# Kernel tuning notes

Hardware: AMD Instinct MI355X
Metric: run time of the kernel (lower is better)

Reference implementation:

```python
import jax, jax.numpy as jnp
import numpy as np

B, S, H, M, T = 64, 512, 768, 512, 26


def setup_inputs() -> dict:
    key = jax.random.key(0)
    ks = jax.random.split(key, 10)
    hidden = jax.random.normal(ks[0], (B, S, H), dtype=jnp.float32)
    W1 = jax.random.normal(ks[1], (M, H), dtype=jnp.float32) * 0.02
    b1 = jnp.zeros((M,), jnp.float32)
    W2 = jax.random.normal(ks[2], (T, M), dtype=jnp.float32) * 0.02
    b2 = jnp.zeros((T,), jnp.float32)
    start_trans = jax.random.normal(ks[3], (T,), dtype=jnp.float32) * 0.1
    end_trans = jax.random.normal(ks[4], (T,), dtype=jnp.float32) * 0.1
    trans = jax.random.normal(ks[5], (T, T), dtype=jnp.float32) * 0.1
    labels = jax.random.randint(ks[6], (B, S), 0, T, dtype=jnp.int32)
    lengths = jax.random.randint(ks[7], (B,), 1, S + 1, dtype=jnp.int32)
    return dict(hidden=hidden, W1=W1, b1=b1, W2=W2, b2=b2,
                start_trans=start_trans, end_trans=end_trans, trans=trans,
                labels=labels, lengths=lengths)


def _crf_nll(emissions, labels, lengths, start_trans, end_trans, trans):
    # emissions: [B,S,T]; labels: [B,S]; lengths: [B]
    maskf = (jnp.arange(S)[None, :] < lengths[:, None]).astype(emissions.dtype)  # [B,S]

    # --- numerator: score of the gold path (torchcrf _compute_score) ---
    emit_gold = jnp.take_along_axis(emissions, labels[..., None], axis=-1)[..., 0]  # [B,S]
    trans_gold = trans[labels[:, :-1], labels[:, 1:]]  # [B,S-1]
    last_tags = jnp.take_along_axis(labels, (lengths - 1)[:, None], axis=1)[:, 0]  # [B]
    numerator = (start_trans[labels[:, 0]] + emit_gold[:, 0]
                 + jnp.sum((trans_gold + emit_gold[:, 1:]) * maskf[:, 1:], axis=1)
                 + end_trans[last_tags])  # [B]

    # --- denominator: log partition via forward algorithm (lax.scan) ---
    alpha0 = start_trans[None, :] + emissions[:, 0]  # [B,T]
    emis_t = jnp.swapaxes(emissions[:, 1:], 0, 1)    # [S-1,B,T]
    mask_t = jnp.swapaxes(maskf[:, 1:] > 0, 0, 1)    # [S-1,B] bool

    def step(alpha, xs):
        emit, m = xs
        # alpha[b,i] + trans[i,j] + emit[b,j] -> logsumexp over i
        nxt = jax.nn.logsumexp(alpha[:, :, None] + trans[None, :, :] + emit[:, None, :], axis=1)
        return jnp.where(m[:, None], nxt, alpha), None

    alpha, _ = jax.lax.scan(step, alpha0, (emis_t, mask_t))
    denominator = jax.nn.logsumexp(alpha + end_trans[None, :], axis=1)  # [B]

    llh = numerator - denominator
    return -jnp.mean(llh)  # loss = -crf(..., reduction='mean')


def reference(hidden, W1, b1, W2, b2, start_trans, end_trans, trans, labels, lengths):
    h = jnp.einsum('bsh,mh->bsm', hidden, W1) + b1      # fc1 (no activation in source)
    emissions = jnp.einsum('bsm,tm->bst', h, W2) + b2   # fc2 -> [B,S,T]
    return _crf_nll(emissions, labels, lengths, start_trans, end_trans, trans)
```

## Files before the change

### kernel.cpp

```cpp
#include <hip/hip_runtime.h>
#include <math.h>

#define Bn 64
#define Sn 512
#define Hn 768
#define Mn 512
#define Tn 26
#define TP 32

#define OFF_BC    0
#define OFF_BFRAG 32
#define OFF_EX    (32 + 12288)
#define EXSZ      ((size_t)Bn*Sn*TP)
#define OFF_ACC   (OFF_EX + EXSZ)
#define OFF_CNT   (OFF_ACC + 1)

typedef __attribute__((ext_vector_type(8)))  short bfrag;
typedef __attribute__((ext_vector_type(4)))  float f32x4;
typedef __attribute__((ext_vector_type(16))) float f32x16;

__device__ __forceinline__ short f2bf(float f) {
    unsigned u = __float_as_uint(f);
    unsigned r = (u + 0x7FFFu + ((u >> 16) & 1u)) >> 16;
    return (short)r;
}
__device__ __forceinline__ unsigned cvtpk(float a, float b) {
    unsigned r;
    asm("v_cvt_pk_bf16_f32 %0, %1, %2" : "=v"(r) : "v"(a), "v"(b));
    return r;
}
__device__ __forceinline__ void pswap(unsigned &a, unsigned &b) {
    asm("v_permlane32_swap_b32 %0, %1" : "+v"(a), "+v"(b));
}
__device__ __forceinline__ bfrag mkfrag(unsigned a, unsigned b, unsigned c, unsigned d) {
    union { unsigned u[4]; bfrag v; } x;
    x.u[0] = a; x.u[1] = b; x.u[2] = c; x.u[3] = d;
    return x.v;
}
__device__ __forceinline__ float rl(float x, int i) {
    return __uint_as_float(__builtin_amdgcn_readlane(__float_as_uint(x), i));
}

__global__ __launch_bounds__(256) void k_prep(const float* __restrict__ W1,
                                              const float* __restrict__ b1,
                                              const float* __restrict__ W2,
                                              const float* __restrict__ b2,
                                              float* __restrict__ ws) {
    const int bx = blockIdx.x;
    const int tid = threadIdx.x;
    if (bx == 48) {
        if (tid == 0) {
            ws[OFF_ACC] = 0.f;
            ((unsigned*)ws)[OFF_CNT] = 0u;
        }
        if (tid < TP) {
            float bcv = 0.f;
            if (tid < Tn) {
                float a0 = 0.f, a1 = 0.f, a2 = 0.f, a3 = 0.f;
                const float4* w2 = reinterpret_cast<const float4*>(W2 + (size_t)tid * Mn);
                const float4* bb = reinterpret_cast<const float4*>(b1);
                for (int m = 0; m < Mn / 4; ++m) {
                    float4 w = w2[m], v = bb[m];
                    a0 = fmaf(w.x, v.x, a0); a1 = fmaf(w.y, v.y, a1);
                    a2 = fmaf(w.z, v.z, a2); a3 = fmaf(w.w, v.w, a3);
                }
                bcv = b2[tid] + (a0 + a1) + (a2 + a3);
            }
            ws[OFF_BC + tid] = bcv;
        }
        return;
    }

    __shared__ float mrg[3][64][8];
    const int lane = tid & 63;
    const int wv   = tid >> 6;
    const int k0   = bx * 16;
    const int colA = lane & 15;
    const int mj   = ((lane >> 4) & 3) * 8;

    f32x4 acc0 = {0.f, 0.f, 0.f, 0.f}, acc1 = {0.f, 0.f, 0.f, 0.f};
    for (int mq = 0; mq < 4; ++mq) {
        const int m0 = wv * 128 + mq * 32;
        bfrag av, bv0, bv1;
#pragma unroll
        for (int j = 0; j < 8; ++j)
            av[j] = f2bf(W1[(size_t)(m0 + mj + j) * Hn + k0 + colA]);
        {
            const float* p = W2 + (size_t)(lane & 15) * Mn + m0 + mj;
            float4 x = *reinterpret_cast<const float4*>(p);
            float4 y = *reinterpret_cast<const float4*>(p + 4);
            bv0 = mkfrag(cvtpk(x.x, x.y), cvtpk(x.z, x.w), cvtpk(y.x, y.y), cvtpk(y.z, y.w));
        }
        {
            int c = 16 + (lane & 15);
            bfrag z = {};
            if (c < Tn) {
                const float* p = W2 + (size_t)c * Mn + m0 + mj;
                float4 x = *reinterpret_cast<const float4*>(p);
                float4 y = *reinterpret_cast<const float4*>(p + 4);
                z = mkfrag(cvtpk(x.x, x.y), cvtpk(x.z, x.w), cvtpk(y.x, y.y), cvtpk(y.z, y.w));
            }
            bv1 = z;
        }
        acc0 = __builtin_amdgcn_mfma_f32_16x16x32_bf16(av, bv0, acc0, 0, 0, 0);
        acc1 = __builtin_amdgcn_mfma_f32_16x16x32_bf16(av, bv1, acc1, 0, 0, 0);
    }

    if (wv > 0) {
#pragma unroll
        for (int i = 0; i < 4; ++i) {
            mrg[wv - 1][lane][i]     = acc0[i];
            mrg[wv - 1][lane][4 + i] = acc1[i];
        }
    }
    __syncthreads();
    if (wv == 0) {
        unsigned short* Bfo = (unsigned short*)(ws + OFF_BFRAG);
#pragma unroll
        for (int i = 0; i < 4; ++i) {
            float v0 = acc0[i] + mrg[0][lane][i]     + mrg[1][lane][i]     + mrg[2][lane][i];
            float v1 = acc1[i] + mrg[0][lane][4 + i] + mrg[1][lane][4 + i] + mrg[2][lane][4 + i];
            int k   = k0 + ((lane >> 4) & 3) * 4 + i;
            int ks2 = k >> 5;
            int fl  = ((k >> 3) & 3) * 16 + (lane & 15);
            Bfo[((size_t)(ks2 * 2 + 0) * 64 + fl) * 8 + (k & 7)] = (unsigned short)f2bf(v0);
            Bfo[((size_t)(ks2 * 2 + 1) * 64 + fl) * 8 + (k & 7)] = (unsigned short)f2bf(v1);
        }
    }
}

#define LOADK(KS, FA, FB, BV0, BV1)                                                        \
    {                                                                                      \
        const float* ap = abase + (KS) * 32;                                               \
        FA = *reinterpret_cast<const float4*>(ap);                                         \
        FB = *reinterpret_cast<const float4*>(ap + 4);                                     \
        BV0 = *reinterpret_cast<const bfrag*>(Bf + ((size_t)((KS) * 2 + 0) * 64 + l) * 8); \
        BV1 = *reinterpret_cast<const bfrag*>(Bf + ((size_t)((KS) * 2 + 1) * 64 + l) * 8); \
    }

__global__ __launch_bounds__(64, 2) void k_gemm(const float* __restrict__ hidden,
                                                const float* __restrict__ ws,
                                                float* __restrict__ Eexp) {
    const int l    = threadIdx.x;
    const int row0 = blockIdx.x * 16;
    const int arow = row0 + (l & 15);
    const int kg   = l >> 4;
    const float* abase = hidden + (size_t)arow * Hn + kg * 8;
    const unsigned short* Bf = (const unsigned short*)(ws + OFF_BFRAG);

    f32x4 acc0 = {0.f, 0.f, 0.f, 0.f}, acc1 = {0.f, 0.f, 0.f, 0.f};

    float4 fa0, fb0, fa1, fb1;
    bfrag bv00, bv01, bv10, bv11;
    LOADK(0, fa0, fb0, bv00, bv01);
    LOADK(1, fa1, fb1, bv10, bv11);

#pragma unroll 1
    for (int ks = 0; ks < 24; ks += 2) {
        float4 ta, tb; bfrag t0, t1;
        if (ks + 2 < 24) LOADK(ks + 2, ta, tb, t0, t1);
        bfrag av = mkfrag(cvtpk(fa0.x, fa0.y), cvtpk(fa0.z, fa0.w),
                          cvtpk(fb0.x, fb0.y), cvtpk(fb0.z, fb0.w));
        acc0 = __builtin_amdgcn_mfma_f32_16x16x32_bf16(av, bv00, acc0, 0, 0, 0);
        acc1 = __builtin_amdgcn_mfma_f32_16x16x32_bf16(av, bv01, acc1, 0, 0, 0);
        fa0 = ta; fb0 = tb; bv00 = t0; bv01 = t1;

        float4 ua, ub; bfrag u0, u1;
        if (ks + 3 < 24) LOADK(ks + 3, ua, ub, u0, u1);
        av = mkfrag(cvtpk(fa1.x, fa1.y), cvtpk(fa1.z, fa1.w),
                    cvtpk(fb1.x, fb1.y), cvtpk(fb1.z, fb1.w));
        acc0 = __builtin_amdgcn_mfma_f32_16x16x32_bf16(av, bv10, acc0, 0, 0, 0);
        acc1 = __builtin_amdgcn_mfma_f32_16x16x32_bf16(av, bv11, acc1, 0, 0, 0);
        fa1 = ua; fb1 = ub; bv10 = u0; bv11 = u1;
    }

    const int c0 = l & 15;
    const int rbase = row0 + kg * 4;
    float bc0 = ws[OFF_BC + c0], bc1 = ws[OFF_BC + 16 + c0];
#pragma unroll
    for (int i = 0; i < 4; ++i) {
        Eexp[(size_t)(rbase + i) * TP + c0]      = __expf(acc0[i] + bc0);
        Eexp[(size_t)(rbase + i) * TP + 16 + c0] = __expf(acc1[i] + bc1);
    }
}

__global__ __launch_bounds__(1024) void k_scan(const float* __restrict__ Eexp,
                                               const float* __restrict__ start_t,
                                               const float* __restrict__ end_t,
                                               const float* __restrict__ trans,
                                               const int* __restrict__ labels,
                                               const int* __restrict__ lengths,
                                               float* __restrict__ accp,
                                               unsigned* __restrict__ cntp,
                                               float* __restrict__ out) {
    __shared__ float Ech[16][32][32];
    __shared__ unsigned Qp[16][16][32];
    const int tid  = threadIdx.x;
    const int b    = blockIdx.x;
    const int len  = lengths[b];
    const int wv   = tid >> 6;
    const int lane = tid & 63;
    const int t    = lane & 31;
    const int h    = lane >> 5;

    {
        const float* Eb = Eexp + (size_t)b * Sn * TP;
        int lr = lane >> 1, hf = lane & 1;
        int s = wv * 32 + 1 + lr; s = s > 511 ? 511 : s;
        const float4* src = reinterpret_cast<const float4*>(Eb + (size_t)s * TP + hf * 16);
        float4* dst = reinterpret_cast<float4*>(&Ech[wv][lr][hf * 16]);
        dst[0] = src[0]; dst[1] = src[1]; dst[2] = src[2]; dst[3] = src[3];
    }
    __syncthreads();

    {
        const int c  = wv;
        const int s0 = c * 32;
        int nact = len - 1 - s0;
        nact = nact < 0 ? 0 : (nact > 32 ? 32 : nact);

        bfrag A0, A1, B0, B1;
#pragma unroll
        for (int j = 0; j < 8; ++j) {
            int k0 = 8 * h + j, k1 = 16 + 8 * h + j;
            A0[j] = (t < Tn && k0 < Tn) ? f2bf(__expf(trans[k0 * Tn + t]) * 0.03125f) : (short)0;
            A1[j] = (t < Tn && k1 < Tn) ? f2bf(__expf(trans[k1 * Tn + t]) * 0.03125f) : (short)0;
            B0[j] = (k0 == t) ? (short)0x3F80 : (short)0;
            B1[j] = (k1 == t) ? (short)0x3F80 : (short)0;
        }

        float qf[16];
#pragma unroll
        for (int r = 0; r < 16; ++r) {
            int row = (r & 3) + 8 * (r >> 2) + 4 * h;
            qf[r] = (row == t) ? 1.f : 0.f;
        }

        for (int j = 0; j < nact; ++j) {
            f32x16 acc = {};
            acc = __builtin_amdgcn_mfma_f32_32x32x16_bf16(A0, B0, acc, 0, 0, 0);
            acc = __builtin_amdgcn_mfma_f32_32x32x16_bf16(A1, B1, acc, 0, 0, 0);
            const float* ep = &Ech[c][j][4 * h];
            float4 e0 = *reinterpret_cast<const float4*>(ep);
            float4 e1 = *reinterpret_cast<const float4*>(ep + 8);
            float4 e2 = *reinterpret_cast<const float4*>(ep + 16);
            float4 e3 = *reinterpret_cast<const float4*>(ep + 24);
            float ev[16];
            ev[0]  = e0.x; ev[1]  = e0.y; ev[2]  = e0.z; ev[3]  = e0.w;
            ev[4]  = e1.x; ev[5]  = e1.y; ev[6]  = e1.z; ev[7]  = e1.w;
            ev[8]  = e2.x; ev[9]  = e2.y; ev[10] = e2.z; ev[11] = e2.w;
            ev[12] = e3.x; ev[13] = e3.y; ev[14] = e3.z; ev[15] = e3.w;
#pragma unroll
            for (int r = 0; r < 16; ++r) qf[r] = acc[r] * ev[r];
            if (j + 1 < nact) {
                unsigned W0 = cvtpk(qf[0],  qf[1]),  W1 = cvtpk(qf[2],  qf[3]);
                unsigned W2 = cvtpk(qf[4],  qf[5]),  W3 = cvtpk(qf[6],  qf[7]);
                unsigned W4 = cvtpk(qf[8],  qf[9]),  W5 = cvtpk(qf[10], qf[11]);
                unsigned W6 = cvtpk(qf[12], qf[13]), W7 = cvtpk(qf[14], qf[15]);
                pswap(W0, W2); pswap(W1, W3); pswap(W4, W6); pswap(W5, W7);
                B0 = mkfrag(W0, W1, W2, W3);
                B1 = mkfrag(W4, W5, W6, W7);
            }
        }

#pragma unroll
        for (int g = 0; g < 4; ++g) {
            unsigned u0 = cvtpk(qf[4*g + 0], qf[4*g + 1]);
            unsigned u1 = cvtpk(qf[4*g + 2], qf[4*g + 3]);
            Qp[c][4*g + 2*h][t]     = u0;
            Qp[c][4*g + 2*h + 1][t] = u1;
        }
    }
    __syncthreads();

    if (wv == 0) {
        float alpha = (t < Tn) ? __expf(start_t[t]) * Eexp[(size_t)b * Sn * TP + t] : 0.f;
        float logZ = 0.f;
        for (int c = 0; c < 16; ++c) {
            float p0 = 0.f, p1 = 0.f, p2 = 0.f, p3 = 0.f;
#pragma unroll
            for (int p = 0; p < 16; p += 2) {
                unsigned ua = Qp[c][p][t];
                unsigned ub = Qp[c][p + 1][t];
                p0 = fmaf(rl(alpha, 2*p    ), __uint_as_float(ua << 16),          p0);
                p1 = fmaf(rl(alpha, 2*p + 1), __uint_as_float(ua & 0xFFFF0000u), p1);
                p2 = fmaf(rl(alpha, 2*p + 2), __uint_as_float(ub << 16),          p2);
                p3 = fmaf(rl(alpha, 2*p + 3), __uint_as_float(ub & 0xFFFF0000u), p3);
            }
            float v = (p0 + p1) + (p2 + p3);
            float C = __uint_as_float(__builtin_amdgcn_readfirstlane(__float_as_uint(v)));
            alpha = v / C;
            logZ += __logf(C);
        }
        float dv = (t < Tn && lane < 32) ? alpha * __expf(end_t[t]) : 0.f;
#pragma unroll
        for (int off = 32; off; off >>= 1) dv += __shfl_xor(dv, off);
        if (lane == 0) {
            float denom = logZ + __logf(dv) + (float)(len - 1) * 3.46573590279973f;
            atomicAdd(accp, -denom);
            __threadfence();
            unsigned old = atomicAdd(cntp, 1u);
            if (old == 2u * Bn - 1u) {
                float tot = atomicAdd(accp, 0.0f);
                out[0] = -tot * (1.0f / 64.0f);
            }
        }
    } else if (wv == 1) {
        const int base = b * Sn;
        float part = 0.f;
        for (int s2 = 1 + lane; s2 < len; s2 += 64) {
            int lp = labels[base + s2 - 1];
            int lc = labels[base + s2];
            int si = s2 - 1;
            part += trans[lp * Tn + lc] + __logf(Ech[si >> 5][si & 31][lc]);
        }
#pragma unroll
        for (int off = 32; off; off >>= 1) part += __shfl_xor(part, off);
        if (lane == 0) {
            int l0 = labels[base], ll = labels[base + len - 1];
            float numer = part + start_t[l0] + __logf(Eexp[(size_t)base * TP + l0]) + end_t[ll];
            atomicAdd(accp, numer);
            __threadfence();
            unsigned old = atomicAdd(cntp, 1u);
            if (old == 2u * Bn - 1u) {
                float tot = atomicAdd(accp, 0.0f);
                out[0] = -tot * (1.0f / 64.0f);
            }
        }
    }
}

extern "C" void kernel_launch(void* const* d_in, const int* in_sizes, int n_in,
                              void* d_out, int out_size, void* d_ws, size_t ws_size,
                              hipStream_t stream) {
    const float* hidden  = (const float*)d_in[0];
    const float* W1      = (const float*)d_in[1];
    const float* b1      = (const float*)d_in[2];
    const float* W2      = (const float*)d_in[3];
    const float* b2      = (const float*)d_in[4];
    const float* start_t = (const float*)d_in[5];
    const float* end_t   = (const float*)d_in[6];
    const float* trans   = (const float*)d_in[7];
    const int*   labels  = (const int*)d_in[8];
    const int*   lengths = (const int*)d_in[9];
    float* ws  = (float*)d_ws;
    float* out = (float*)d_out;

    hipLaunchKernelGGL(k_prep, dim3(49), dim3(256), 0, stream, W1, b1, W2, b2, ws);
    hipLaunchKernelGGL(k_gemm, dim3(2048), dim3(64), 0, stream, hidden, ws, ws + OFF_EX);
    hipLaunchKernelGGL(k_scan, dim3(64), dim3(1024), 0, stream, ws + OFF_EX, start_t, end_t,
                       trans, labels, lengths, ws + OFF_ACC,
                       (unsigned*)(ws + OFF_CNT), out);
}
```

Measured before the change: 53.62 us.

## Deepen GEMM prefetch pipeline to four stages and parallelize bias fold reduction

The GEMM main loop now keeps four k-steps of A and B fragments in flight instead of two, issuing each next load right after the MFMA that consumes the previous buffer. Past the end of K it reloads step 0 unconditionally rather than branching. This is meant to hide global-load latency for a memory-bound, low-occupancy kernel, at the cost of more registers and some redundant tail loads. Separately, the bias-fold block in the prep kernel spreads the W2·b1 dot products across all 256 threads and combines them with a shuffle and shared memory, where before only 26 threads did serial loops.

```diff
diff --git a/kernel.cpp b/kernel.cpp
--- a/kernel.cpp
+++ b/kernel.cpp
@@ -49,23 +49,37 @@
     const int bx = blockIdx.x;
     const int tid = threadIdx.x;
     if (bx == 48) {
+        __shared__ float part[4][32];
         if (tid == 0) {
             ws[OFF_ACC] = 0.f;
             ((unsigned*)ws)[OFF_CNT] = 0u;
         }
+        const int c = tid & 31;
+        const int w = tid >> 6;
+        const int cl = (tid >> 5) & 1;
+        float a0 = 0.f, a1 = 0.f;
+        if (c < Tn) {
+            const int m0 = w * 128 + cl * 64;
+            const float4* w2 = reinterpret_cast<const float4*>(W2 + (size_t)c * Mn + m0);
+            const float4* bb = reinterpret_cast<const float4*>(b1 + m0);
+#pragma unroll
+            for (int m = 0; m < 16; m += 2) {
+                float4 wA = w2[m], vA = bb[m];
+                float4 wB = w2[m + 1], vB = bb[m + 1];
+                a0 = fmaf(wA.x, vA.x, a0); a0 = fmaf(wA.y, vA.y, a0);
+                a0 = fmaf(wA.z, vA.z, a0); a0 = fmaf(wA.w, vA.w, a0);
+                a1 = fmaf(wB.x, vB.x, a1); a1 = fmaf(wB.y, vB.y, a1);
+                a1 = fmaf(wB.z, vB.z, a1); a1 = fmaf(wB.w, vB.w, a1);
+            }
+        }
+        float h0 = a0 + a1;
+        float h1 = __shfl_xor(h0, 32);
+        if ((tid & 63) < 32) part[w][c] = h0 + h1;
+        __syncthreads();
         if (tid < TP) {
             float bcv = 0.f;
-            if (tid < Tn) {
-                float a0 = 0.f, a1 = 0.f, a2 = 0.f, a3 = 0.f;
-                const float4* w2 = reinterpret_cast<const float4*>(W2 + (size_t)tid * Mn);
-                const float4* bb = reinterpret_cast<const float4*>(b1);
-                for (int m = 0; m < Mn / 4; ++m) {
-                    float4 w = w2[m], v = bb[m];
-                    a0 = fmaf(w.x, v.x, a0); a1 = fmaf(w.y, v.y, a1);
-                    a2 = fmaf(w.z, v.z, a2); a3 = fmaf(w.w, v.w, a3);
-                }
-                bcv = b2[tid] + (a0 + a1) + (a2 + a3);
-            }
+            if (tid < Tn)
+                bcv = b2[tid] + ((part[0][tid] + part[1][tid]) + (part[2][tid] + part[3][tid]));
             ws[OFF_BC + tid] = bcv;
         }
         return;
@@ -136,6 +150,15 @@
         FB = *reinterpret_cast<const float4*>(ap + 4);                                     \
         BV0 = *reinterpret_cast<const bfrag*>(Bf + ((size_t)((KS) * 2 + 0) * 64 + l) * 8); \
         BV1 = *reinterpret_cast<const bfrag*>(Bf + ((size_t)((KS) * 2 + 1) * 64 + l) * 8); \
+    }
+#define STEP(FA, FB, BV0, BV1, KN)                                                \
+    {                                                                             \
+        bfrag av = mkfrag(cvtpk(FA.x, FA.y), cvtpk(FA.z, FA.w),                   \
+                          cvtpk(FB.x, FB.y), cvtpk(FB.z, FB.w));                  \
+        acc0 = __builtin_amdgcn_mfma_f32_16x16x32_bf16(av, BV0, acc0, 0, 0, 0);   \
+        acc1 = __builtin_amdgcn_mfma_f32_16x16x32_bf16(av, BV1, acc1, 0, 0, 0);   \
+        int kp = (KN) < 24 ? (KN) : 0;                                            \
+        LOADK(kp, FA, FB, BV0, BV1);                                              \
     }
 
 __global__ __launch_bounds__(64, 2) void k_gemm(const float* __restrict__ hidden,
@@ -150,28 +173,19 @@
 
     f32x4 acc0 = {0.f, 0.f, 0.f, 0.f}, acc1 = {0.f, 0.f, 0.f, 0.f};
 
-    float4 fa0, fb0, fa1, fb1;
-    bfrag bv00, bv01, bv10, bv11;
+    float4 fa0, fb0, fa1, fb1, fa2, fb2, fa3, fb3;
+    bfrag bv00, bv01, bv10, bv11, bv20, bv21, bv30, bv31;
     LOADK(0, fa0, fb0, bv00, bv01);
     LOADK(1, fa1, fb1, bv10, bv11);
+    LOADK(2, fa2, fb2, bv20, bv21);
+    LOADK(3, fa3, fb3, bv30, bv31);
 
 #pragma unroll 1
-    for (int ks = 0; ks < 24; ks += 2) {
-        float4 ta, tb; bfrag t0, t1;
-        if (ks + 2 < 24) LOADK(ks + 2, ta, tb, t0, t1);
-        bfrag av = mkfrag(cvtpk(fa0.x, fa0.y), cvtpk(fa0.z, fa0.w),
-                          cvtpk(fb0.x, fb0.y), cvtpk(fb0.z, fb0.w));
-        acc0 = __builtin_amdgcn_mfma_f32_16x16x32_bf16(av, bv00, acc0, 0, 0, 0);
-        acc1 = __builtin_amdgcn_mfma_f32_16x16x32_bf16(av, bv01, acc1, 0, 0, 0);
-        fa0 = ta; fb0 = tb; bv00 = t0; bv01 = t1;
-
-        float4 ua, ub; bfrag u0, u1;
-        if (ks + 3 < 24) LOADK(ks + 3, ua, ub, u0, u1);
-        av = mkfrag(cvtpk(fa1.x, fa1.y), cvtpk(fa1.z, fa1.w),
-                    cvtpk(fb1.x, fb1.y), cvtpk(fb1.z, fb1.w));
-        acc0 = __builtin_amdgcn_mfma_f32_16x16x32_bf16(av, bv10, acc0, 0, 0, 0);
-        acc1 = __builtin_amdgcn_mfma_f32_16x16x32_bf16(av, bv11, acc1, 0, 0, 0);
-        fa1 = ua; fb1 = ub; bv10 = u0; bv11 = u1;
+    for (int ks = 0; ks < 24; ks += 4) {
+        STEP(fa0, fb0, bv00, bv01, ks + 4);
+        STEP(fa1, fb1, bv10, bv11, ks + 5);
+        STEP(fa2, fb2, bv20, bv21, ks + 6);
+        STEP(fa3, fb3, bv30, bv31, ks + 7);
     }
 
     const int c0 = l & 15;
```

Measured after the change: 75.69 us. 1.41x slower.
